# Optimization experiments

Measured on AMD Instinct MI355X. Metric: run time of the kernel, lower is better.

## Reference

```python
import jax, jax.numpy as jnp
import numpy as np

NUM_SITES = 64
BOND_DIM = 64
PHYS_DIM = 2
BATCH = 8192
INIT_STD = 0.125  # 1/sqrt(bond_dim)
EPS_AMP = 1e-12
EPS_LOG = 1e-30


def setup_inputs() -> dict:
    key = jax.random.key(0)
    k_cfg, k_l, k_b, k_r = jax.random.split(key, 4)
    configurations = jax.random.randint(k_cfg, (BATCH, NUM_SITES), 0, PHYS_DIM, dtype=jnp.int32)
    left = jax.random.normal(k_l, (PHYS_DIM, BOND_DIM), dtype=jnp.float32) * INIT_STD
    bulk = jax.random.normal(k_b, (NUM_SITES - 2, BOND_DIM, PHYS_DIM, BOND_DIM), dtype=jnp.float32) * INIT_STD
    right = jax.random.normal(k_r, (BOND_DIM, PHYS_DIM), dtype=jnp.float32) * INIT_STD
    return {"configurations": configurations, "left": left, "bulk": bulk, "right": right}


def _psi(configurations, left, bulk, right):
    # configurations: [B, S] int; left: [d, D]; bulk: [S-2, D, d, D]; right: [D, d]
    B = configurations.shape[0]
    env0 = left[configurations[:, 0]]  # [B, D]
    cfg_mid = configurations[:, 1:-1].T  # [S-2, B]

    def step(env, xs):
        site_t, idx = xs  # site_t: [D, d, D], idx: [B]
        D = site_t.shape[0]
        # env @ site (contract left bond), then gather the per-sample physical slice
        tmp = (env @ site_t.reshape(D, -1)).reshape(B, PHYS_DIM, D)  # [B, d, D]
        env = jnp.take_along_axis(tmp, idx[:, None, None], axis=1)[:, 0, :]  # [B, D]
        return env, None

    env, _ = jax.lax.scan(step, env0, (bulk, cfg_mid))
    cols = jnp.take(right, configurations[:, -1], axis=1).T  # [B, D]
    return jnp.sum(env * cols, axis=1)  # [B]


def _log_norm(left, bulk, right):
    env0 = left.T @ left  # [D, D]  (real dtype -> conj trivial)

    def step(carry, site_t):
        env, log_scale = carry
        sm = jnp.transpose(site_t, (1, 0, 2))  # [d, D, D]
        env = jnp.einsum('pdi,de,pej->ij', sm, env, sm)  # sum_p A_p^H env A_p
        scale = jnp.maximum(jnp.max(jnp.abs(env)), EPS_LOG)
        return (env / scale, log_scale + jnp.log(scale)), None

    (env, log_scale), _ = jax.lax.scan(step, (env0, jnp.zeros((), left.dtype)), bulk)
    z = jnp.sum(right * (env @ right))
    return jnp.log(jnp.maximum(z, EPS_LOG)) + log_scale


def reference(configurations, left, bulk, right):
    psi = _psi(configurations, left, bulk, right)
    abs_sq = jnp.maximum(psi * psi, EPS_AMP)
    log_z = _log_norm(left, bulk, right)
    nll = -(jnp.log(abs_sq) - log_z)
    return jnp.mean(nll)
```

## Files before the change

kernel.cpp:

```cpp
#include <hip/hip_runtime.h>
#include <math.h>

#define NBULK 62
#define SB    72

typedef __attribute__((ext_vector_type(8))) short bf8_t;
typedef __attribute__((ext_vector_type(4))) float f4_t;
typedef __attribute__((ext_vector_type(16))) float f16v_t;

#define MFMA16(a, b, c) __builtin_amdgcn_mfma_f32_16x16x32_bf16((a), (b), (c), 0, 0, 0)
#define MFMA32(a, b, c) __builtin_amdgcn_mfma_f32_32x32x16_bf16((a), (b), (c), 0, 0, 0)

__device__ __forceinline__ unsigned short f2bf(float f) {
    unsigned int u = __float_as_uint(f);
    return (unsigned short)((u + 0x7FFFu + ((u >> 16) & 1u)) >> 16);
}
__device__ __forceinline__ float bf2f(unsigned short h) {
    return __uint_as_float(((unsigned int)h) << 16);
}
__device__ __forceinline__ unsigned cvtpk(float lo, float hi) {
    unsigned r;
    asm("v_cvt_pk_bf16_f32 %0, %1, %2" : "=v"(r) : "v"(lo), "v"(hi));
    return r;
}

__device__ __forceinline__ void gload16(const void* g, void* l) {
    __builtin_amdgcn_global_load_lds(
        (const __attribute__((address_space(1))) unsigned int*)g,
        (__attribute__((address_space(3))) unsigned int*)l, 16, 0, 0);
}

#define WS_E_OFF   1024
#define WS_B_OFF   6144
#define WS_BT_OFF  45056
#define WS_MR_OFF  1060864


extern "C" __global__ __launch_bounds__(256)
void mps_precompute(const float* __restrict__ bulkG,
                    unsigned short* __restrict__ BTg,
                    unsigned short* __restrict__ MRg,
                    float* __restrict__ wsF)
{
    __shared__ unsigned short BTl[8192];
    __shared__ unsigned short MRl[8192];
    const int s = blockIdx.x, tid = threadIdx.x;
    if (s == 0 && tid == 0) {
        wsF[0] = 0.f; wsF[1] = 0.f; wsF[2] = 0.f; wsF[3] = 0.f;
    }
    const float4* src = (const float4*)(bulkG + (size_t)s * 8192);
    for (int c = 0; c < 8; ++c) {
        int idx = tid + c * 256;
        float4 v = src[idx];
        int f  = idx * 4;
        int kk = f >> 7;
        int p  = (f >> 6) & 1;
        int j  = f & 63;
        unsigned short b0 = f2bf(v.x), b1 = f2bf(v.y), b2 = f2bf(v.z), b3 = f2bf(v.w);
        int n = p * 64 + kk;
        int off = n * 64 + (((j >> 3) ^ (n & 7)) << 3) + (j & 7);
        MRl[off + 0] = b0; MRl[off + 1] = b1; MRl[off + 2] = b2; MRl[off + 3] = b3;
        unsigned short bb[4] = {b0, b1, b2, b3};
        #pragma unroll
        for (int t2 = 0; t2 < 4; ++t2) {
            int n2 = p * 64 + j + t2;
            BTl[n2 * 64 + (((kk >> 3) ^ (n2 & 7)) << 3) + (kk & 7)] = bb[t2];
        }
    }
    __syncthreads();
    const uint4* bt4 = (const uint4*)BTl;
    const uint4* mr4 = (const uint4*)MRl;
    uint4* btg = (uint4*)(BTg + (size_t)s * 8192);
    uint4* mrg = (uint4*)(MRg + (size_t)s * 8192);
    for (int c = 0; c < 4; ++c) {
        int idx = tid + c * 256;
        btg[idx] = bt4[idx];
        mrg[idx] = mr4[idx];
    }
}

__device__ __forceinline__ void psi_phase(
    uint4 (&R)[16], int tt, unsigned short* env, const char* BTb,
    const int (&off)[4], unsigned selLo, unsigned selHi,
    int s, int hi, int e7, const f16v_t& Z)
{
    bf8_t benv[4];
    #pragma unroll
    for (int ks = 0; ks < 4; ++ks)
        benv[ks] = *(const bf8_t*)((const char*)env + s * 128 + (((ks * 2 + hi) ^ e7) << 4));
    unsigned sbit = (tt + 1 < 32) ? (selLo >> (tt + 1)) : (selHi >> (tt - 31));
    const bool takeB = (sbit & 1u) != 0u;
    #pragma unroll
    for (int jt = 0; jt < 2; ++jt) {
        f16v_t a0 = Z, a1 = Z;
        #pragma unroll
        for (int ks = 0; ks < 4; ++ks) {
            a0 = MFMA32(*(const bf8_t*)&R[jt * 4 + ks],     benv[ks], a0);
            a1 = MFMA32(*(const bf8_t*)&R[8 + jt * 4 + ks], benv[ks], a1);
        }
        #pragma unroll
        for (int b = 0; b < 4; ++b) {
            float v0 = takeB ? a1[4 * b + 0] : a0[4 * b + 0];
            float v1 = takeB ? a1[4 * b + 1] : a0[4 * b + 1];
            float v2 = takeB ? a1[4 * b + 2] : a0[4 * b + 2];
            float v3 = takeB ? a1[4 * b + 3] : a0[4 * b + 3];
            uint2 w;
            w.x = cvtpk(v0, v1);
            w.y = cvtpk(v2, v3);
            *(uint2*)((char*)env + s * 128 + (((jt * 4 + b) ^ e7) << 4) + hi * 8) = w;
        }
    }
    if (tt + 2 < NBULK) {
        const char* tb = BTb + (size_t)(tt + 2) * 16384;
        #pragma unroll
        for (int p = 0; p < 2; ++p)
            #pragma unroll
            for (int jt = 0; jt < 2; ++jt)
                #pragma unroll
                for (int ks = 0; ks < 4; ++ks)
                    R[p * 8 + jt * 4 + ks] =
                        *(const uint4*)(tb + p * 8192 + jt * 4096 + off[ks]);
    }
}

extern "C" __global__ __launch_bounds__(256)
void mps_main(const int* __restrict__ cfgG, const float* __restrict__ leftG,
              const float* __restrict__ rightG, float* __restrict__ wsF,
              const unsigned short* __restrict__ BTg,
              const unsigned short* __restrict__ MRg)
{
    extern __shared__ char smem[];
    unsigned short* smem16 = (unsigned short*)smem;
    const int tid  = threadIdx.x;
    const int bid  = blockIdx.x;
    const int wv   = tid >> 6;
    const int lane = tid & 63;

    if (bid >= 2) {
        if (wv >= 2) return;
        const int s  = lane & 31;
        const int hi = lane >> 5;
        const int e7 = lane & 7;
        unsigned short* env = smem16 + wv * 2048;
        const int s0 = (bid - 2) * 64 + wv * 32;

        int off[4];
        #pragma unroll
        for (int ks = 0; ks < 4; ++ks)
            off[ks] = s * 128 + (((ks * 2 + hi) ^ e7) << 4);

        const char* BTb = (const char*)BTg;
        uint4 ra[16], rb[16];
        #pragma unroll
        for (int p = 0; p < 2; ++p)
            #pragma unroll
            for (int jt = 0; jt < 2; ++jt)
                #pragma unroll
                for (int ks = 0; ks < 4; ++ks) {
                    ra[p * 8 + jt * 4 + ks] = *(const uint4*)(BTb + p * 8192 + jt * 4096 + off[ks]);
                    rb[p * 8 + jt * 4 + ks] = *(const uint4*)(BTb + 16384 + p * 8192 + jt * 4096 + off[ks]);
                }

        unsigned mbits = 0;
        {
            const int4* crow = (const int4*)(cfgG + (size_t)(s0 + s) * 64 + hi * 32);
            #pragma unroll
            for (int c = 0; c < 8; ++c) {
                int4 v = crow[c];
                mbits |= (unsigned)(v.x & 1) << (c * 4 + 0);
                mbits |= (unsigned)(v.y & 1) << (c * 4 + 1);
                mbits |= (unsigned)(v.z & 1) << (c * 4 + 2);
                mbits |= (unsigned)(v.w & 1) << (c * 4 + 3);
            }
        }
        unsigned other = __shfl_xor(mbits, 32);
        unsigned selLo = hi ? other : mbits;
        unsigned selHi = hi ? mbits : other;

        {
            const float* lp = leftG + (selLo & 1u) * 64 + hi * 32;
            #pragma unroll
            for (int gg = 0; gg < 4; ++gg) {
                float4 a = *(const float4*)(lp + gg * 8);
                float4 b = *(const float4*)(lp + gg * 8 + 4);
                uint4 w;
                w.x = (unsigned)f2bf(a.x) | ((unsigned)f2bf(a.y) << 16);
                w.y = (unsigned)f2bf(a.z) | ((unsigned)f2bf(a.w) << 16);
                w.z = (unsigned)f2bf(b.x) | ((unsigned)f2bf(b.y) << 16);
                w.w = (unsigned)f2bf(b.z) | ((unsigned)f2bf(b.w) << 16);
                int g = hi * 4 + gg;
                *(uint4*)((char*)env + s * 128 + ((g ^ e7) << 4)) = w;
            }
        }

        const f16v_t Z = {0.f};
        for (int t = 0; t < NBULK; t += 2) {
            psi_phase(ra, t,     env, BTb, off, selLo, selHi, s, hi, e7, Z);
            psi_phase(rb, t + 1, env, BTb, off, selLo, selHi, s, hi, e7, Z);
        }

        {
            int selL = (selHi >> 31) & 1;
            float psum = 0.f;
            #pragma unroll
            for (int gg = 0; gg < 4; ++gg) {
                int g = hi * 4 + gg;
                bf8_t e = *(const bf8_t*)((const char*)env + s * 128 + ((g ^ e7) << 4));
                #pragma unroll
                for (int j = 0; j < 8; ++j)
                    psum = fmaf(bf2f((unsigned short)e[j]), rightG[(g * 8 + j) * 2 + selL], psum);
            }
            psum += __shfl_xor(psum, 32);
            float lp = logf(fmaxf(psum * psum, 1e-12f));
            if (hi) lp = 0.f;
            #pragma unroll
            for (int o = 1; o < 64; o <<= 1) lp += __shfl_xor(lp, o);
            if (lane == 0) atomicAdd(&wsF[0], lp);
        }
    } else {
        unsigned short* Ebf = smem16;
        unsigned short* St0 = Ebf + 64 * SB;
        unsigned short* St1 = St0 + 64 * SB;
        unsigned short* Ms0 = St1 + 64 * SB;
        unsigned short* Ms1 = Ms0 + 8192;
        float* wred = (float*)(Ms1 + 8192);

        const int quad = lane >> 4;
        const int ln   = lane & 15;
        const bool fwd = (bid == 0);
        const unsigned short* srcbase = fwd ? BTg : MRg;
        {
            int i = tid >> 2, jq = tid & 3;
            for (int jj = 0; jj < 16; ++jj) {
                int j = jq * 16 + jj;
                float v;
                if (fwd) v = leftG[i] * leftG[j] + leftG[64 + i] * leftG[64 + j];
                else     v = rightG[i * 2] * rightG[j * 2] + rightG[i * 2 + 1] * rightG[j * 2 + 1];
                Ebf[i * SB + j] = f2bf(v);
            }
        }
        {
            int st = fwd ? 0 : 61;
            const char* g = (const char*)(srcbase + (size_t)st * 8192);
            for (int c = 0; c < 4; ++c) {
                int chunk = wv * 4 + c;
                gload16(g + chunk * 1024 + (size_t)lane * 16, (char*)Ms0 + chunk * 1024);
            }
        }
        float lsum = 0.f;
        const int p   = wv >> 1;
        const int ntb = (wv & 1) * 2;
        const int mta = (wv >> 1) * 2;
        const int nta = (wv & 1) * 2;
        unsigned short* Stp = p ? St1 : St0;

        for (int k = 0; k < 31; ++k) {
            __syncthreads();
            unsigned short* M = (k & 1) ? Ms1 : Ms0;
            if (k + 1 < 31) {
                int sn = fwd ? (k + 1) : (61 - (k + 1));
                const char* g = (const char*)(srcbase + (size_t)sn * 8192);
                char* l = (char*)((k & 1) ? Ms0 : Ms1);
                for (int c = 0; c < 4; ++c) {
                    int chunk = wv * 4 + c;
                    gload16(g + chunk * 1024 + (size_t)lane * 16, l + chunk * 1024);
                }
            }
            float inv = 1.f;
            if (k > 0) {
                const float* wp = wred + ((k - 1) & 1) * 4;
                float mm = fmaxf(fmaxf(wp[0], wp[1]), fmaxf(wp[2], wp[3]));
                float sc = fmaxf(mm, 1e-30f);
                inv = 1.f / sc;
                if (tid == 0) lsum += logf(sc);
            }
            {
                bf8_t Af2[4][2];
                #pragma unroll
                for (int mt = 0; mt < 4; ++mt)
                    #pragma unroll
                    for (int h = 0; h < 2; ++h)
                        Af2[mt][h] = *(const bf8_t*)(Ebf + (mt * 16 + ln) * SB + h * 32 + quad * 8);
                #pragma unroll
                for (int c = 0; c < 2; ++c) {
                    int nt = ntb + c;
                    int row = p * 64 + nt * 16 + ln;
                    bf8_t B0 = *(const bf8_t*)(M + row * 64 + (((0 + quad) ^ (ln & 7)) << 3));
                    bf8_t B1 = *(const bf8_t*)(M + row * 64 + (((4 + quad) ^ (ln & 7)) << 3));
                    #pragma unroll
                    for (int mt = 0; mt < 4; ++mt) {
                        f4_t a = {0.f, 0.f, 0.f, 0.f};
                        a = MFMA16(Af2[mt][0], B0, a);
                        a = MFMA16(Af2[mt][1], B1, a);
                        ushort4 pk;
                        pk.x = f2bf(a[0]); pk.y = f2bf(a[1]); pk.z = f2bf(a[2]); pk.w = f2bf(a[3]);
                        *(ushort4*)(Stp + (nt * 16 + ln) * SB + mt * 16 + quad * 4) = pk;
                    }
                }
            }
            asm volatile("s_waitcnt lgkmcnt(0)" ::: "memory");
            __builtin_amdgcn_s_barrier();
            __builtin_amdgcn_sched_barrier(0);
            {
                bf8_t Aw[2][2][2], Bw[2][2][2];
                #pragma unroll
                for (int pp = 0; pp < 2; ++pp)
                    #pragma unroll
                    for (int mi = 0; mi < 2; ++mi)
                        #pragma unroll
                        for (int h = 0; h < 2; ++h)
                            Aw[pp][mi][h] = *(const bf8_t*)(M + (pp * 64 + (mta + mi) * 16 + ln) * 64
                                                              + (((h * 4 + quad) ^ (ln & 7)) << 3));
                #pragma unroll
                for (int pp = 0; pp < 2; ++pp)
                    #pragma unroll
                    for (int ni = 0; ni < 2; ++ni)
                        #pragma unroll
                        for (int h = 0; h < 2; ++h)
                            Bw[pp][ni][h] = *(const bf8_t*)((pp ? St1 : St0)
                                                            + ((nta + ni) * 16 + ln) * SB + h * 32 + quad * 8);
                float mx = 0.f;
                #pragma unroll
                for (int mi = 0; mi < 2; ++mi)
                    #pragma unroll
                    for (int ni = 0; ni < 2; ++ni) {
                        f4_t a = {0.f, 0.f, 0.f, 0.f};
                        #pragma unroll
                        for (int pp = 0; pp < 2; ++pp)
                            #pragma unroll
                            for (int h = 0; h < 2; ++h)
                                a = MFMA16(Aw[pp][mi][h], Bw[pp][ni][h], a);
                        float x0 = a[0] * inv, x1 = a[1] * inv, x2 = a[2] * inv, x3 = a[3] * inv;
                        mx = fmaxf(mx, fmaxf(fmaxf(fabsf(x0), fabsf(x1)), fmaxf(fabsf(x2), fabsf(x3))));
                        ushort4 pk;
                        pk.x = f2bf(x0); pk.y = f2bf(x1); pk.z = f2bf(x2); pk.w = f2bf(x3);
                        *(ushort4*)(Ebf + ((nta + ni) * 16 + ln) * SB + (mta + mi) * 16 + quad * 4) = pk;
                    }
                #pragma unroll
                for (int off2 = 32; off2 > 0; off2 >>= 1)
                    mx = fmaxf(mx, __shfl_xor(mx, off2));
                if (lane == 0) wred[(k & 1) * 4 + wv] = mx;
            }
        }
        __syncthreads();
        float* dst = wsF + (fwd ? WS_E_OFF : WS_B_OFF);
        for (int c = 0; c < 16; ++c) {
            int idx = tid + c * 256;
            dst[idx] = bf2f(Ebf[(idx >> 6) * SB + (idx & 63)]);
        }
        if (tid == 0) wsF[fwd ? 1 : 2] = lsum;
    }
}

extern "C" __global__ void mps_finalize(const float* __restrict__ wsF, float* __restrict__ out)
{
    const int lane = threadIdx.x;
    const float* E  = wsF + WS_E_OFF;
    const float* Bm = wsF + WS_B_OFF;
    float a = 0.f;
    #pragma unroll 8
    for (int j = 0; j < 64; ++j)
        a = fmaf(E[lane * 64 + j], Bm[lane * 64 + j], a);
    #pragma unroll
    for (int off = 32; off > 0; off >>= 1)
        a += __shfl_down(a, off);
    if (lane == 0) {
        const float z = fmaxf(a, 1e-30f);
        const float log_z = logf(z) + wsF[1] + wsF[2];
        out[0] = log_z - wsF[0] * (1.0f / 8192.0f);
    }
}

extern "C" void kernel_launch(void* const* d_in, const int* in_sizes, int n_in,
                              void* d_out, int out_size, void* d_ws, size_t ws_size,
                              hipStream_t stream)
{
    const int*   cfg   = (const int*)d_in[0];
    const float* left  = (const float*)d_in[1];
    const float* bulk  = (const float*)d_in[2];
    const float* right = (const float*)d_in[3];
    float* wsF = (float*)d_ws;
    unsigned short* BTg = (unsigned short*)((char*)d_ws + WS_BT_OFF);
    unsigned short* MRg = (unsigned short*)((char*)d_ws + WS_MR_OFF);

    mps_precompute<<<dim3(62), dim3(256), 0, stream>>>(bulk, BTg, MRg, wsF);
    mps_main<<<dim3(130), dim3(256), 60480, stream>>>(cfg, left, right, wsF, BTg, MRg);
    mps_finalize<<<dim3(1), dim3(64), 0, stream>>>(wsF, (float*)d_out);
}
```

Before: 119.0 us.

## Keep psi environment in MFMA16 registers using fragment-ordered bulk layout

Adds a third precomputed bulk layout stored in the 16x16x32 MFMA fragment order. The psi chain now switches from 32x32 MFMAs to 16x16 ones and packs each step's accumulator straight into the next B operand in registers, so the per-step LDS write and read of the environment go away. All four waves per block now run, 16 samples each, instead of two waves with 32 each. The cost is one more precompute buffer, more fragment global loads per step, and a small change to the barrier and finalize access pattern.

New measurement: 117.9 us. No clear change (-0.9%).

```diff
diff --git a/kernel.cpp b/kernel.cpp
--- a/kernel.cpp
+++ b/kernel.cpp
@@ -6,10 +6,8 @@
 
 typedef __attribute__((ext_vector_type(8))) short bf8_t;
 typedef __attribute__((ext_vector_type(4))) float f4_t;
-typedef __attribute__((ext_vector_type(16))) float f16v_t;
 
 #define MFMA16(a, b, c) __builtin_amdgcn_mfma_f32_16x16x32_bf16((a), (b), (c), 0, 0, 0)
-#define MFMA32(a, b, c) __builtin_amdgcn_mfma_f32_32x32x16_bf16((a), (b), (c), 0, 0, 0)
 
 __device__ __forceinline__ unsigned short f2bf(float f) {
     unsigned int u = __float_as_uint(f);
@@ -34,16 +32,19 @@
 #define WS_B_OFF   6144
 #define WS_BT_OFF  45056
 #define WS_MR_OFF  1060864
+#define WS_NFF_OFF 2076672
 
 
 extern "C" __global__ __launch_bounds__(256)
 void mps_precompute(const float* __restrict__ bulkG,
                     unsigned short* __restrict__ BTg,
                     unsigned short* __restrict__ MRg,
+                    unsigned short* __restrict__ NFfG,
                     float* __restrict__ wsF)
 {
     __shared__ unsigned short BTl[8192];
     __shared__ unsigned short MRl[8192];
+    __shared__ unsigned short Ffl[8192];
     const int s = blockIdx.x, tid = threadIdx.x;
     if (s == 0 && tid == 0) {
         wsF[0] = 0.f; wsF[1] = 0.f; wsF[2] = 0.f; wsF[3] = 0.f;
@@ -55,79 +56,84 @@
         int f  = idx * 4;
         int kk = f >> 7;
         int p  = (f >> 6) & 1;
-        int j  = f & 63;
+        int j0 = f & 63;
         unsigned short b0 = f2bf(v.x), b1 = f2bf(v.y), b2 = f2bf(v.z), b3 = f2bf(v.w);
+        unsigned short bb[4] = {b0, b1, b2, b3};
         int n = p * 64 + kk;
-        int off = n * 64 + (((j >> 3) ^ (n & 7)) << 3) + (j & 7);
+        int off = n * 64 + (((j0 >> 3) ^ (n & 7)) << 3) + (j0 & 7);
         MRl[off + 0] = b0; MRl[off + 1] = b1; MRl[off + 2] = b2; MRl[off + 3] = b3;
-        unsigned short bb[4] = {b0, b1, b2, b3};
+        int qf = (kk >> 2) & 3, rf = kk & 3, mf = kk >> 4;
+        int ksf = mf >> 1, jjf = (mf & 1) * 4 + rf;
         #pragma unroll
         for (int t2 = 0; t2 < 4; ++t2) {
-            int n2 = p * 64 + j + t2;
+            int j = j0 + t2;
+            int n2 = p * 64 + j;
             BTl[n2 * 64 + (((kk >> 3) ^ (n2 & 7)) << 3) + (kk & 7)] = bb[t2];
+            int tf = j >> 4, lnf = j & 15;
+            Ffl[((p * 4 + tf) * 2 + ksf) * 512 + (qf * 16 + lnf) * 8 + jjf] = bb[t2];
         }
     }
     __syncthreads();
     const uint4* bt4 = (const uint4*)BTl;
     const uint4* mr4 = (const uint4*)MRl;
+    const uint4* ff4 = (const uint4*)Ffl;
     uint4* btg = (uint4*)(BTg + (size_t)s * 8192);
     uint4* mrg = (uint4*)(MRg + (size_t)s * 8192);
+    uint4* ffg = (uint4*)(NFfG + (size_t)s * 8192);
     for (int c = 0; c < 4; ++c) {
         int idx = tid + c * 256;
         btg[idx] = bt4[idx];
         mrg[idx] = mr4[idx];
-    }
-}
-
-__device__ __forceinline__ void psi_phase(
-    uint4 (&R)[16], int tt, unsigned short* env, const char* BTb,
-    const int (&off)[4], unsigned selLo, unsigned selHi,
-    int s, int hi, int e7, const f16v_t& Z)
-{
-    bf8_t benv[4];
-    #pragma unroll
-    for (int ks = 0; ks < 4; ++ks)
-        benv[ks] = *(const bf8_t*)((const char*)env + s * 128 + (((ks * 2 + hi) ^ e7) << 4));
-    unsigned sbit = (tt + 1 < 32) ? (selLo >> (tt + 1)) : (selHi >> (tt - 31));
-    const bool takeB = (sbit & 1u) != 0u;
-    #pragma unroll
-    for (int jt = 0; jt < 2; ++jt) {
-        f16v_t a0 = Z, a1 = Z;
+        ffg[idx] = ff4[idx];
+    }
+}
+
+__device__ __forceinline__ void pfetch(uint4 (&F)[16], const char* tb, int l16)
+{
+    #pragma unroll
+    for (int i = 0; i < 16; ++i)
+        F[i] = *(const uint4*)(tb + i * 1024 + l16);
+}
+
+__device__ __forceinline__ void pstep(f4_t (&a)[2][4], const uint4 (&F)[16],
+                                      const bf8_t (&B)[2])
+{
+    #pragma unroll
+    for (int p = 0; p < 2; ++p)
         #pragma unroll
-        for (int ks = 0; ks < 4; ++ks) {
-            a0 = MFMA32(*(const bf8_t*)&R[jt * 4 + ks],     benv[ks], a0);
-            a1 = MFMA32(*(const bf8_t*)&R[8 + jt * 4 + ks], benv[ks], a1);
-        }
-        #pragma unroll
-        for (int b = 0; b < 4; ++b) {
-            float v0 = takeB ? a1[4 * b + 0] : a0[4 * b + 0];
-            float v1 = takeB ? a1[4 * b + 1] : a0[4 * b + 1];
-            float v2 = takeB ? a1[4 * b + 2] : a0[4 * b + 2];
-            float v3 = takeB ? a1[4 * b + 3] : a0[4 * b + 3];
-            uint2 w;
-            w.x = cvtpk(v0, v1);
-            w.y = cvtpk(v2, v3);
-            *(uint2*)((char*)env + s * 128 + (((jt * 4 + b) ^ e7) << 4) + hi * 8) = w;
-        }
-    }
-    if (tt + 2 < NBULK) {
-        const char* tb = BTb + (size_t)(tt + 2) * 16384;
+        for (int mt = 0; mt < 4; ++mt) { f4_t z = {0.f, 0.f, 0.f, 0.f}; a[p][mt] = z; }
+    #pragma unroll
+    for (int ks = 0; ks < 2; ++ks)
         #pragma unroll
         for (int p = 0; p < 2; ++p)
             #pragma unroll
-            for (int jt = 0; jt < 2; ++jt)
-                #pragma unroll
-                for (int ks = 0; ks < 4; ++ks)
-                    R[p * 8 + jt * 4 + ks] =
-                        *(const uint4*)(tb + p * 8192 + jt * 4096 + off[ks]);
-    }
-}
-
-extern "C" __global__ __launch_bounds__(256)
+            for (int mt = 0; mt < 4; ++mt)
+                a[p][mt] = MFMA16(*(const bf8_t*)&F[(p * 4 + mt) * 2 + ks], B[ks], a[p][mt]);
+}
+
+__device__ __forceinline__ void ppack(bf8_t (&B)[2], const f4_t (&a)[2][4], bool takeB)
+{
+    #pragma unroll
+    for (int ks = 0; ks < 2; ++ks) {
+        unsigned w[4];
+        #pragma unroll
+        for (int d = 0; d < 4; ++d) {
+            int mt = 2 * ks + (d >> 1), r = (d & 1) * 2;
+            float x0 = takeB ? a[1][mt][r]     : a[0][mt][r];
+            float x1 = takeB ? a[1][mt][r + 1] : a[0][mt][r + 1];
+            w[d] = cvtpk(x0, x1);
+        }
+        uint4 u = {w[0], w[1], w[2], w[3]};
+        B[ks] = *(const bf8_t*)&u;
+    }
+}
+
+extern "C" __global__ __launch_bounds__(256, 1)
 void mps_main(const int* __restrict__ cfgG, const float* __restrict__ leftG,
               const float* __restrict__ rightG, float* __restrict__ wsF,
               const unsigned short* __restrict__ BTg,
-              const unsigned short* __restrict__ MRg)
+              const unsigned short* __restrict__ MRg,
+              const unsigned short* __restrict__ NFfG)
 {
     extern __shared__ char smem[];
     unsigned short* smem16 = (unsigned short*)smem;
@@ -135,88 +141,79 @@
     const int bid  = blockIdx.x;
     const int wv   = tid >> 6;
     const int lane = tid & 63;
+    const int ln   = lane & 15, q = lane >> 4;
+    const int l16  = lane * 16;
 
     if (bid >= 2) {
-        if (wv >= 2) return;
-        const int s  = lane & 31;
-        const int hi = lane >> 5;
-        const int e7 = lane & 7;
-        unsigned short* env = smem16 + wv * 2048;
-        const int s0 = (bid - 2) * 64 + wv * 32;
-
-        int off[4];
-        #pragma unroll
-        for (int ks = 0; ks < 4; ++ks)
-            off[ks] = s * 128 + (((ks * 2 + hi) ^ e7) << 4);
-
-        const char* BTb = (const char*)BTg;
-        uint4 ra[16], rb[16];
-        #pragma unroll
-        for (int p = 0; p < 2; ++p)
-            #pragma unroll
-            for (int jt = 0; jt < 2; ++jt)
-                #pragma unroll
-                for (int ks = 0; ks < 4; ++ks) {
-                    ra[p * 8 + jt * 4 + ks] = *(const uint4*)(BTb + p * 8192 + jt * 4096 + off[ks]);
-                    rb[p * 8 + jt * 4 + ks] = *(const uint4*)(BTb + 16384 + p * 8192 + jt * 4096 + off[ks]);
+        const char* NF = (const char*)NFfG;
+        uint4 Fa[16], Fb[16];
+        pfetch(Fa, NF, l16);
+        pfetch(Fb, NF + 16384, l16);
+        const int s0 = (bid - 2) * 64 + wv * 16;
+        unsigned part = 0;
+        {
+            const int4* crow = (const int4*)(cfgG + (size_t)(s0 + ln) * 64 + q * 16);
+            #pragma unroll
+            for (int c = 0; c < 4; ++c) {
+                int4 v = crow[c];
+                part |= (unsigned)(v.x & 1) << (c * 4 + 0);
+                part |= (unsigned)(v.y & 1) << (c * 4 + 1);
+                part |= (unsigned)(v.z & 1) << (c * 4 + 2);
+                part |= (unsigned)(v.w & 1) << (c * 4 + 3);
+            }
+        }
+        unsigned pp   = __shfl_xor(part, 16);
+        unsigned comb = (q & 1) ? (pp | (part << 16)) : (part | (pp << 16));
+        unsigned selLo = __shfl(comb, ln);
+        unsigned selHi = __shfl(comb, ln + 32);
+
+        bf8_t B[2];
+        {
+            const float* lp = leftG + (selLo & 1u) * 64;
+            #pragma unroll
+            for (int ks = 0; ks < 2; ++ks) {
+                unsigned w[4];
+                #pragma unroll
+                for (int d = 0; d < 4; ++d) {
+                    int k0 = 16 * (2 * ks + (d >> 1)) + 4 * q + 2 * (d & 1);
+                    w[d] = (unsigned)f2bf(lp[k0]) | ((unsigned)f2bf(lp[k0 + 1]) << 16);
                 }
-
-        unsigned mbits = 0;
-        {
-            const int4* crow = (const int4*)(cfgG + (size_t)(s0 + s) * 64 + hi * 32);
-            #pragma unroll
-            for (int c = 0; c < 8; ++c) {
-                int4 v = crow[c];
-                mbits |= (unsigned)(v.x & 1) << (c * 4 + 0);
-                mbits |= (unsigned)(v.y & 1) << (c * 4 + 1);
-                mbits |= (unsigned)(v.z & 1) << (c * 4 + 2);
-                mbits |= (unsigned)(v.w & 1) << (c * 4 + 3);
-            }
-        }
-        unsigned other = __shfl_xor(mbits, 32);
-        unsigned selLo = hi ? other : mbits;
-        unsigned selHi = hi ? mbits : other;
-
-        {
-            const float* lp = leftG + (selLo & 1u) * 64 + hi * 32;
-            #pragma unroll
-            for (int gg = 0; gg < 4; ++gg) {
-                float4 a = *(const float4*)(lp + gg * 8);
-                float4 b = *(const float4*)(lp + gg * 8 + 4);
-                uint4 w;
-                w.x = (unsigned)f2bf(a.x) | ((unsigned)f2bf(a.y) << 16);
-                w.y = (unsigned)f2bf(a.z) | ((unsigned)f2bf(a.w) << 16);
-                w.z = (unsigned)f2bf(b.x) | ((unsigned)f2bf(b.y) << 16);
-                w.w = (unsigned)f2bf(b.z) | ((unsigned)f2bf(b.w) << 16);
-                int g = hi * 4 + gg;
-                *(uint4*)((char*)env + s * 128 + ((g ^ e7) << 4)) = w;
-            }
-        }
-
-        const f16v_t Z = {0.f};
-        for (int t = 0; t < NBULK; t += 2) {
-            psi_phase(ra, t,     env, BTb, off, selLo, selHi, s, hi, e7, Z);
-            psi_phase(rb, t + 1, env, BTb, off, selLo, selHi, s, hi, e7, Z);
-        }
-
-        {
-            int selL = (selHi >> 31) & 1;
+                uint4 u = {w[0], w[1], w[2], w[3]};
+                B[ks] = *(const bf8_t*)&u;
+            }
+        }
+        f4_t a[2][4];
+        #define SELBIT(i) ((bool)((((i) < 32) ? (selLo >> (i)) : (selHi >> ((i) - 32))) & 1u))
+        for (int t = 0; t < 60; t += 2) {
+            pstep(a, Fa, B);
+            pfetch(Fa, NF + (size_t)(t + 2) * 16384, l16);
+            ppack(B, a, SELBIT(t + 1));
+            pstep(a, Fb, B);
+            pfetch(Fb, NF + (size_t)(t + 3) * 16384, l16);
+            ppack(B, a, SELBIT(t + 2));
+        }
+        pstep(a, Fa, B);
+        ppack(B, a, SELBIT(61));
+        pstep(a, Fb, B);
+        {
+            bool tb2 = SELBIT(62);
+            int selL = (int)(selHi >> 31) & 1;
             float psum = 0.f;
             #pragma unroll
-            for (int gg = 0; gg < 4; ++gg) {
-                int g = hi * 4 + gg;
-                bf8_t e = *(const bf8_t*)((const char*)env + s * 128 + ((g ^ e7) << 4));
-                #pragma unroll
-                for (int j = 0; j < 8; ++j)
-                    psum = fmaf(bf2f((unsigned short)e[j]), rightG[(g * 8 + j) * 2 + selL], psum);
-            }
+            for (int mt = 0; mt < 4; ++mt)
+                #pragma unroll
+                for (int r = 0; r < 4; ++r) {
+                    float v = tb2 ? a[1][mt][r] : a[0][mt][r];
+                    psum = fmaf(v, rightG[(16 * mt + 4 * q + r) * 2 + selL], psum);
+                }
+            psum += __shfl_xor(psum, 16);
             psum += __shfl_xor(psum, 32);
-            float lp = logf(fmaxf(psum * psum, 1e-12f));
-            if (hi) lp = 0.f;
-            #pragma unroll
-            for (int o = 1; o < 64; o <<= 1) lp += __shfl_xor(lp, o);
-            if (lane == 0) atomicAdd(&wsF[0], lp);
-        }
+            float lp2 = (lane < 16) ? logf(fmaxf(psum * psum, 1e-12f)) : 0.f;
+            #pragma unroll
+            for (int o = 1; o < 64; o <<= 1) lp2 += __shfl_xor(lp2, o);
+            if (lane == 0) atomicAdd(&wsF[0], lp2);
+        }
+        #undef SELBIT
     } else {
         unsigned short* Ebf = smem16;
         unsigned short* St0 = Ebf + 64 * SB;
@@ -225,8 +222,7 @@
         unsigned short* Ms1 = Ms0 + 8192;
         float* wred = (float*)(Ms1 + 8192);
 
-        const int quad = lane >> 4;
-        const int ln   = lane & 15;
+        const int quad = q;
         const bool fwd = (bid == 0);
         const unsigned short* srcbase = fwd ? BTg : MRg;
         {
@@ -298,9 +294,7 @@
                     }
                 }
             }
-            asm volatile("s_waitcnt lgkmcnt(0)" ::: "memory");
-            __builtin_amdgcn_s_barrier();
-            __builtin_amdgcn_sched_barrier(0);
+            __syncthreads();
             {
                 bf8_t Aw[2][2][2], Bw[2][2][2];
                 #pragma unroll
@@ -360,7 +354,7 @@
     float a = 0.f;
     #pragma unroll 8
     for (int j = 0; j < 64; ++j)
-        a = fmaf(E[lane * 64 + j], Bm[lane * 64 + j], a);
+        a = fmaf(E[j * 64 + lane], Bm[j * 64 + lane], a);
     #pragma unroll
     for (int off = 32; off > 0; off >>= 1)
         a += __shfl_down(a, off);
@@ -382,8 +376,10 @@
     float* wsF = (float*)d_ws;
     unsigned short* BTg = (unsigned short*)((char*)d_ws + WS_BT_OFF);
     unsigned short* MRg = (unsigned short*)((char*)d_ws + WS_MR_OFF);
-
-    mps_precompute<<<dim3(62), dim3(256), 0, stream>>>(bulk, BTg, MRg, wsF);
-    mps_main<<<dim3(130), dim3(256), 60480, stream>>>(cfg, left, right, wsF, BTg, MRg);
+    unsigned short* NFf = (unsigned short*)((char*)d_ws + WS_NFF_OFF);
+
+    mps_precompute<<<dim3(62), dim3(256), 0, stream>>>(bulk, BTg, MRg, NFf, wsF);
+    mps_main<<<dim3(130), dim3(256), 60480, stream>>>(cfg, left, right, wsF,
+                                                      BTg, MRg, NFf);
     mps_finalize<<<dim3(1), dim3(64), 0, stream>>>(wsF, (float*)d_out);
 }
```
